# Performance work log

Measured on AMD Instinct MI355X. Metric: run time of the kernel, lower is better.

## Reference

```python
import jax, jax.numpy as jnp
import numpy as np

BN_EPS = 1e-5


def _conv2d(x, w, b, pad):
    # x: [B,C,H,W], w: [O,I,kh,kw] (OIHW)
    y = jax.lax.conv_general_dilated(
        x, w, window_strides=(1, 1), padding=[(pad, pad), (pad, pad)],
        dimension_numbers=('NCHW', 'OIHW', 'NCHW'))
    return y + b[None, :, None, None]


def setup_inputs() -> dict:
    key = jax.random.key(0)
    ks = jax.random.split(key, 4)
    B, C, D, H, W = 8, 256, 1, 64, 64
    dm = 256
    x = jax.random.normal(ks[0], (B, C, D, H, W), dtype=jnp.float32)
    wq = jax.random.normal(ks[1], (dm, dm, 1, 1), dtype=jnp.float32) * 0.05
    bq = jnp.zeros((dm,), jnp.float32)
    wkv = jax.random.normal(ks[2], (2 * dm, dm, 3, 3), dtype=jnp.float32) * 0.05
    bkv = jnp.zeros((2 * dm,), jnp.float32)
    gamma = jnp.ones((dm,), jnp.float32)
    beta = jnp.zeros((dm,), jnp.float32)
    return {"x": x, "wq": wq, "bq": bq, "wkv": wkv, "bkv": bkv,
            "gamma": gamma, "beta": beta}


def reference(x, wq, bq, wkv, bkv, gamma, beta):
    B = x.shape[0]
    H, W = x.shape[-2], x.shape[-1]
    xc = x.reshape(B, -1, H, W)            # 'b c d h w -> b (c d) h w'
    dm = xc.shape[1]
    q = jax.nn.relu(_conv2d(xc, wq, bq, 0))       # [B,dm,H,W]
    kv = jax.nn.relu(_conv2d(xc, wkv, bkv, 1))    # [B,2dm,H,W]
    k, v = jnp.split(kv, 2, axis=1)

    def tok(t):  # 'b c x y -> b (x y) c'
        return t.transpose(0, 2, 3, 1).reshape(B, H * W, dm)

    qt, kt, vt = tok(q), tok(k), tok(v)
    sim = jnp.einsum('bid,bjd->bij', qt, kt)       # [B,N,N]
    A = jax.nn.softmax(sim / jnp.sqrt(jnp.float32(dm)), axis=-1)
    r = jnp.einsum('bij,bjd->bid', A, vt)          # [B,N,dm]
    r = r.reshape(B, H, W, dm).transpose(0, 3, 1, 2)  # 'b (x y) c -> b c x y'
    y = r + xc
    # BatchNorm2d, training mode: batch stats over (B,H,W), biased variance
    mean = jnp.mean(y, axis=(0, 2, 3), keepdims=True)
    var = jnp.var(y, axis=(0, 2, 3), keepdims=True)
    out = (y - mean) * jax.lax.rsqrt(var + BN_EPS)
    out = out * gamma[None, :, None, None] + beta[None, :, None, None]
    return out
```

## Files before the change

### kernel.cpp

```cpp
#include <hip/hip_runtime.h>


typedef __attribute__((ext_vector_type(8))) short bf16x8;
typedef __attribute__((ext_vector_type(4))) float f32x4;
typedef __attribute__((ext_vector_type(8))) unsigned short u16x8;

__device__ inline unsigned short f2bf(float f) {
  union { float f; unsigned u; } c; c.f = f;
  unsigned u = c.u;
  return (unsigned short)((u + 0x7fffu + ((u >> 16) & 1u)) >> 16);
}

__device__ inline unsigned cvtpk(float lo, float hi) {
  unsigned r;
  asm("v_cvt_pk_bf16_f32 %0, %1, %2" : "=v"(r) : "v"(lo), "v"(hi));
  return r;
}

__device__ inline void dma16(const void* g, void* l) {
  __builtin_amdgcn_global_load_lds(
      (const __attribute__((address_space(1))) unsigned int*)g,
      (__attribute__((address_space(3))) unsigned int*)l, 16, 0, 0);
}

__global__ __launch_bounds__(256) void k_xt(
    const float* __restrict__ x, ushort* __restrict__ xt)
{
  const int b = blockIdx.z, ci0 = blockIdx.y * 64, gx = blockIdx.x;
  const int t = threadIdx.x;
  ushort* img = xt + (size_t)b * 4224 * 256;
  if (gx >= 64) {
    int r0 = (gx == 64) ? 0 : 4160;
#pragma unroll
    for (int k = 0; k < 2; ++k) {
      int idx = t + k * 256;
      int r = idx >> 3, u = idx & 7;
      u16x8 z = (u16x8)0;
      *(u16x8*)&img[(size_t)(r0 + r) * 256 + ci0 + u * 8] = z;
    }
    return;
  }
  const int n0 = gx * 64;
  __shared__ ushort tl[64][65];
  {
    const float* xb = x + ((size_t)b * 256 + ci0) * 4096 + n0;
    int i = t >> 2, j0 = (t & 3) * 16;
#pragma unroll
    for (int jj = 0; jj < 16; jj += 4) {
      float4 v = *(const float4*)&xb[(size_t)i * 4096 + j0 + jj];
      tl[j0 + jj + 0][i] = f2bf(v.x);
      tl[j0 + jj + 1][i] = f2bf(v.y);
      tl[j0 + jj + 2][i] = f2bf(v.z);
      tl[j0 + jj + 3][i] = f2bf(v.w);
    }
  }
  __syncthreads();
  {
    int j = t >> 3, u = t & 7;
#pragma unroll
    for (int k = 0; k < 2; ++k) {
      int jr = j + k * 32;
      ushort tmp[8];
#pragma unroll
      for (int e = 0; e < 8; ++e) tmp[e] = tl[jr][u * 8 + e];
      *(u16x8*)&img[(size_t)(64 + n0 + jr) * 256 + ci0 + u * 8] = *(u16x8*)tmp;
    }
  }
}

__global__ __launch_bounds__(256) void k_wprep(
    const float* __restrict__ w, ushort* __restrict__ wt, int ntaps, int nco)
{
  const int co = blockIdx.x;
  const int t = threadIdx.x;
  __shared__ float ws[2304];
  const int tot = 256 * ntaps;
  for (int i = t; i < tot; i += 256) ws[i] = w[(size_t)co * tot + i];
  __syncthreads();
  for (int tap = 0; tap < ntaps; ++tap)
    wt[((size_t)tap * nco + co) * 256 + t] = f2bf(ws[t * ntaps + tap]);
}

__global__ __launch_bounds__(256, 2) void k_conv(
    const ushort* __restrict__ xt, const ushort* __restrict__ wt,
    const float* __restrict__ bias, ushort* __restrict__ outT,
    ushort* __restrict__ outV, int ntaps, int nco, float oscale)
{
  extern __shared__ unsigned char smem[];
  ushort* As = (ushort*)smem;
  ushort* Bs = (ushort*)(smem + 20640);
  __shared__ float bias_s[256];

  const int t = threadIdx.x, lane = t & 63, wv = t >> 6;
  const int wm = wv >> 1, wn = wv & 1;
  const int qc = lane & 15, grp = lane >> 4;
  const int b = blockIdx.z, n0 = blockIdx.x * 128, co0 = blockIdx.y * 256;
  const bool nchw = (outV != nullptr) && (blockIdx.y == 1);
  const ushort* img = xt + (size_t)b * 4224 * 256 + (size_t)64 * 256;

  bias_s[t] = bias[co0 + t];

  f32x4 acc[4][8];
#pragma unroll
  for (int mi = 0; mi < 4; ++mi)
#pragma unroll
    for (int ni = 0; ni < 8; ++ni) acc[mi][ni] = f32x4{0.f, 0.f, 0.f, 0.f};

  for (int c8 = 0; c8 < 8; ++c8) {
    const int ci0 = c8 * 32;
    __syncthreads();
#pragma unroll
    for (int k = 0; k < 5; ++k) {
      int idx = t + k * 256;
      if (idx < 1032) {
        int r = idx >> 2, u = idx & 3;
        int n = n0 + r - 65;
        n = min(max(n, -64), 4159);
        u16x8 v = *(const u16x8*)&img[(size_t)n * 256 + ci0 + u * 8];
        *(u16x8*)&As[r * 40 + u * 8] = v;
      }
    }
    for (int tap = 0; tap < ntaps; ++tap) {
      const int dy = (ntaps == 9) ? (tap / 3 - 1) : 0;
      const int dx = (ntaps == 9) ? (tap % 3 - 1) : 0;
      const int off = dy * 64 + dx;
      __syncthreads();
      const ushort* wrow = wt + ((size_t)tap * nco + co0) * 256 + ci0;
#pragma unroll
      for (int k = 0; k < 4; ++k) {
        int idx = t + k * 256;
        int r = idx >> 2, u = idx & 3;
        *(u16x8*)&Bs[r * 40 + u * 8] = *(const u16x8*)&wrow[(size_t)r * 256 + u * 8];
      }
      __syncthreads();
      bf16x8 bf[8];
#pragma unroll
      for (int ni = 0; ni < 8; ++ni)
        bf[ni] = *(const bf16x8*)&Bs[(wn * 128 + ni * 16 + qc) * 40 + grp * 8];
#pragma unroll
      for (int mi = 0; mi < 4; ++mi) {
        int ar = wm * 64 + mi * 16 + qc + off + 65;
        bf16x8 af = *(const bf16x8*)&As[ar * 40 + grp * 8];
        if (dx < 0 && mi == 0 && qc == 0)  af = (bf16x8)0;
        if (dx > 0 && mi == 3 && qc == 15) af = (bf16x8)0;
#pragma unroll
        for (int ni = 0; ni < 8; ++ni)
          acc[mi][ni] = __builtin_amdgcn_mfma_f32_16x16x32_bf16(af, bf[ni], acc[mi][ni], 0, 0, 0);
      }
    }
  }

  __syncthreads();
  if (!nchw) {
    ushort (*olds)[264] = (ushort(*)[264])smem;
#pragma unroll
    for (int mi = 0; mi < 4; ++mi) {
      int p = wm * 64 + mi * 16 + grp * 4;
#pragma unroll
      for (int ni = 0; ni < 8; ++ni) {
        int c = wn * 128 + ni * 16 + qc;
        float bv = bias_s[c];
#pragma unroll
        for (int r = 0; r < 4; ++r)
          olds[p + r][c] = f2bf(fmaxf(acc[mi][ni][r] + bv, 0.f) * oscale);
      }
    }
    __syncthreads();
    ushort* dst = outT + ((size_t)b * 4096 + n0) * 256;
#pragma unroll
    for (int k = 0; k < 16; ++k) {
      int idx = t + k * 256;
      int r = idx >> 5, u = idx & 31;
      *(u16x8*)&dst[(size_t)r * 256 + u * 8] = *(const u16x8*)&olds[r][u * 8];
    }
  } else {
    ushort (*oldsT)[136] = (ushort(*)[136])smem;
#pragma unroll
    for (int mi = 0; mi < 4; ++mi) {
      int p = wm * 64 + mi * 16 + grp * 4;
#pragma unroll
      for (int ni = 0; ni < 8; ++ni) {
        int c = wn * 128 + ni * 16 + qc;
        float bv = bias_s[c];
        ushort4 pk;
        pk.x = f2bf(fmaxf(acc[mi][ni][0] + bv, 0.f) * oscale);
        pk.y = f2bf(fmaxf(acc[mi][ni][1] + bv, 0.f) * oscale);
        pk.z = f2bf(fmaxf(acc[mi][ni][2] + bv, 0.f) * oscale);
        pk.w = f2bf(fmaxf(acc[mi][ni][3] + bv, 0.f) * oscale);
        *(ushort4*)&oldsT[c][p] = pk;
      }
    }
    __syncthreads();
    ushort* dst = outV + (size_t)b * 256 * 4096 + n0;
#pragma unroll
    for (int k = 0; k < 16; ++k) {
      int idx = t + k * 256;
      int c = idx >> 4, u = idx & 15;
      *(u16x8*)&dst[(size_t)c * 4096 + u * 8] = *(const u16x8*)&oldsT[c][u * 8];
    }
  }
}

__global__ __launch_bounds__(512, 2) void k_attn(
    const ushort* __restrict__ q_t, const ushort* __restrict__ k_t,
    const ushort* __restrict__ v_t, const float* __restrict__ x,
    float* __restrict__ y, float* __restrict__ gstat)
{
  extern __shared__ unsigned char smem[];
  ushort* kbf0 = (ushort*)smem;
  ushort* kbf1 = (ushort*)(smem + 32768);
  ushort* vbf0 = (ushort*)(smem + 65536);
  ushort* vbf1 = (ushort*)(smem + 98304);
  ushort* pl   = (ushort*)(smem + 131072);

  const int tid = threadIdx.x, lane = tid & 63, w = tid >> 6;
  const int grp = lane >> 4, qc = lane & 15, xr = qc & 7;
  const int b = blockIdx.y, q0 = blockIdx.x * 128;
  const int wbase = tid & ~63;

  int offk[4], offv[4];
#pragma unroll
  for (int k = 0; k < 4; ++k) {
    int i = k * 512 + tid;
    int j = i >> 5, s = i & 31;
    offk[k] = j * 256 + ((s ^ (j & 7)) << 3);
    int d = i >> 3, s2 = i & 7;
    offv[k] = d * 4096 + ((s2 ^ (d & 7)) << 3);
  }
  const ushort* kT = k_t + (size_t)b * 4096 * 256;
  const ushort* vT = v_t + (size_t)b * 256 * 4096;

  bf16x8 qf[8];
  {
    const ushort* qrow = q_t + ((size_t)b * 4096 + q0 + w * 16 + qc) * 256;
#pragma unroll
    for (int dc = 0; dc < 8; ++dc)
      qf[dc] = *(const bf16x8*)&qrow[dc * 32 + grp * 8];
  }

  f32x4 o[16];
#pragma unroll
  for (int dt = 0; dt < 16; ++dt) o[dt] = f32x4{0.f, 0.f, 0.f, 0.f};
  float m_run = -1e30f, lp = 0.f;

  auto stage = [&](const ushort* kp, const ushort* vp, ushort* kb, ushort* vb) {
#pragma unroll
    for (int k = 0; k < 4; ++k)
      dma16(kp + offk[k], kb + (size_t)(k * 512 + wbase) * 8);
#pragma unroll
    for (int k = 0; k < 4; ++k)
      dma16(vp + offv[k], vb + (size_t)(k * 512 + wbase) * 8);
  };

  stage(kT, vT, kbf0, vbf0);
  kT += 16384; vT += 64;
  asm volatile("s_waitcnt vmcnt(0)" ::: "memory");
  __syncthreads();

  ushort* prow = pl + (size_t)(w * 16 + qc) * 64;
  int po[4], pslot[2];
#pragma unroll
  for (int kt = 0; kt < 4; ++kt)
    po[kt] = (((2 * kt + (grp >> 1)) ^ xr) << 3) + ((grp & 1) << 2);
#pragma unroll
  for (int kc = 0; kc < 2; ++kc)
    pslot[kc] = ((kc * 4 + grp) ^ xr) << 3;

  for (int t = 0; t < 64; ++t) {
    ushort* kb = (t & 1) ? kbf1 : kbf0;
    ushort* vb = (t & 1) ? vbf1 : vbf0;
    if (t < 63) {
      stage(kT, vT, (t & 1) ? kbf0 : kbf1, (t & 1) ? vbf0 : vbf1);
      kT += 16384; vT += 64;
    }

    f32x4 st[4];
    __builtin_amdgcn_s_setprio(1);
#pragma unroll
    for (int kt = 0; kt < 4; ++kt) {
      const int row = (kt * 16 + qc) * 256;
      bf16x8 ka8[8];
#pragma unroll
      for (int dc = 0; dc < 8; ++dc)
        ka8[dc] = *(const bf16x8*)&kb[row + (((dc * 4 + grp) ^ xr) << 3)];
      f32x4 a = f32x4{0.f, 0.f, 0.f, 0.f};
#pragma unroll
      for (int dc = 0; dc < 8; ++dc)
        a = __builtin_amdgcn_mfma_f32_16x16x32_bf16(ka8[dc], qf[dc], a, 0, 0, 0);
      st[kt] = a;
    }
    __builtin_amdgcn_s_setprio(0);

    float pmax = fmaxf(
        fmaxf(fmaxf(st[0][0], st[0][1]), fmaxf(st[0][2], st[0][3])),
        fmaxf(fmaxf(st[1][0], st[1][1]), fmaxf(st[1][2], st[1][3])));
    pmax = fmaxf(pmax, fmaxf(
        fmaxf(fmaxf(st[2][0], st[2][1]), fmaxf(st[2][2], st[2][3])),
        fmaxf(fmaxf(st[3][0], st[3][1]), fmaxf(st[3][2], st[3][3]))));
    pmax = fmaxf(pmax, __shfl_xor(pmax, 16));
    pmax = fmaxf(pmax, __shfl_xor(pmax, 32));
    if (pmax - m_run > 11.5f) {
      float mn = fmaxf(m_run, pmax);
      float al = exp2f(m_run - mn);
      m_run = mn; lp *= al;
#pragma unroll
      for (int dt = 0; dt < 16; ++dt) {
        o[dt][0] *= al; o[dt][1] *= al; o[dt][2] *= al; o[dt][3] *= al;
      }
    }
#pragma unroll
    for (int kt = 0; kt < 4; ++kt) {
      float p0 = exp2f(st[kt][0] - m_run);
      float p1 = exp2f(st[kt][1] - m_run);
      float p2 = exp2f(st[kt][2] - m_run);
      float p3 = exp2f(st[kt][3] - m_run);
      lp += (p0 + p1) + (p2 + p3);
      uint2 pk = { cvtpk(p0, p1), cvtpk(p2, p3) };
      *(uint2*)&prow[po[kt]] = pk;
    }

    bf16x8 pb0 = *(const bf16x8*)&prow[pslot[0]];
    bf16x8 pb1 = *(const bf16x8*)&prow[pslot[1]];
    bf16x8 vaA[8], vaB[8];
#pragma unroll
    for (int j = 0; j < 8; ++j) {
      int dt = j >> 1;
      vaA[j] = *(const bf16x8*)&vb[(dt * 16 + qc) * 64 + pslot[j & 1]];
    }
    __builtin_amdgcn_s_setprio(1);
#pragma unroll
    for (int bt = 0; bt < 4; ++bt) {
      const bf16x8* cur = (bt & 1) ? vaB : vaA;
      bf16x8* nxt = (bt & 1) ? vaA : vaB;
      if (bt < 3) {
#pragma unroll
        for (int j = 0; j < 8; ++j) {
          int dt = (bt + 1) * 4 + (j >> 1);
          nxt[j] = *(const bf16x8*)&vb[(dt * 16 + qc) * 64 + pslot[j & 1]];
        }
      }
#pragma unroll
      for (int j2 = 0; j2 < 4; ++j2) {
        int dt = bt * 4 + j2;
        o[dt] = __builtin_amdgcn_mfma_f32_16x16x32_bf16(cur[2 * j2],     pb0, o[dt], 0, 0, 0);
        o[dt] = __builtin_amdgcn_mfma_f32_16x16x32_bf16(cur[2 * j2 + 1], pb1, o[dt], 0, 0, 0);
      }
    }
    __builtin_amdgcn_s_setprio(0);

    asm volatile("s_waitcnt vmcnt(0)" ::: "memory");
    __syncthreads();
  }

  lp += __shfl_xor(lp, 16);
  lp += __shfl_xor(lp, 32);
  float inv = 1.f / lp;

  float (*obuf)[132] = (float(*)[132])smem;
  float* bnacc = (float*)(smem + 135168);
  bnacc[tid] = 0.f;
#pragma unroll
  for (int dt = 0; dt < 16; ++dt)
#pragma unroll
    for (int r = 0; r < 4; ++r)
      obuf[dt * 16 + grp * 4 + r][w * 16 + qc] = o[dt][r] * inv;
  __syncthreads();

  const float* xb = x + (size_t)b * 256 * 4096 + q0;
  float*       yb = y + (size_t)b * 256 * 4096 + q0;
  for (int i = tid; i < 8192; i += 512) {
    int c = i >> 5, f4 = (i & 31) << 2;
    float4 xr4 = *(const float4*)&xb[(size_t)c * 4096 + f4];
    float4 rv = *(const float4*)&obuf[c][f4];
    rv.x += xr4.x; rv.y += xr4.y; rv.z += xr4.z; rv.w += xr4.w;
    *(float4*)&yb[(size_t)c * 4096 + f4] = rv;
    float ls1 = (rv.x + rv.y) + (rv.z + rv.w);
    float ls2 = (rv.x * rv.x + rv.y * rv.y) + (rv.z * rv.z + rv.w * rv.w);
    atomicAdd(&bnacc[c], ls1);
    atomicAdd(&bnacc[256 + c], ls2);
  }
  __syncthreads();
  if (tid < 256) {
    atomicAdd(&gstat[tid], bnacc[tid]);
    atomicAdd(&gstat[256 + tid], bnacc[256 + tid]);
  }
}

__global__ __launch_bounds__(256) void k_bnfin(
    const float* __restrict__ gstat, const float* __restrict__ gamma,
    const float* __restrict__ beta, float* __restrict__ scale,
    float* __restrict__ shift)
{
  const int c = threadIdx.x;
  float mean = gstat[c] * (1.f / 32768.f);
  float var  = gstat[256 + c] * (1.f / 32768.f) - mean * mean;
  float inv  = rsqrtf(var + 1e-5f);
  float g = gamma[c] * inv;
  scale[c] = g;
  shift[c] = beta[c] - mean * g;
}

__global__ __launch_bounds__(256) void k_bnapply(
    float* __restrict__ y, const float* __restrict__ scale,
    const float* __restrict__ shift)
{
  const int total4 = 8 * 256 * 1024;
  for (int i = blockIdx.x * 256 + threadIdx.x; i < total4; i += gridDim.x * 256) {
    int c = (i >> 10) & 255;
    float sc = scale[c], sh = shift[c];
    float4 v = ((const float4*)y)[i];
    v.x = fmaf(v.x, sc, sh);
    v.y = fmaf(v.y, sc, sh);
    v.z = fmaf(v.z, sc, sh);
    v.w = fmaf(v.w, sc, sh);
    ((float4*)y)[i] = v;
  }
}

extern "C" void kernel_launch(void* const* d_in, const int* in_sizes, int n_in,
                              void* d_out, int out_size, void* d_ws, size_t ws_size,
                              hipStream_t stream) {
  const float* x     = (const float*)d_in[0];
  const float* wq    = (const float*)d_in[1];
  const float* bq    = (const float*)d_in[2];
  const float* wkv   = (const float*)d_in[3];
  const float* bkv   = (const float*)d_in[4];
  const float* gamma = (const float*)d_in[5];
  const float* beta  = (const float*)d_in[6];
  float* out = (float*)d_out;

  ushort* xt  = (ushort*)d_ws;
  ushort* wt3 = xt  + (size_t)8650752;
  ushort* wt1 = wt3 + (size_t)1179648;
  ushort* q_t = wt1 + (size_t)65536;
  ushort* k_t = q_t + (size_t)8388608;
  ushort* v_t = k_t + (size_t)8388608;
  float* scale = (float*)(v_t + (size_t)8388608);
  float* shift = scale + 256;
  float* gstat = shift + 256;

  hipMemsetAsync(gstat, 0, 2048, stream);

  k_xt<<<dim3(66, 4, 8), 256, 0, stream>>>(x, xt);
  k_wprep<<<dim3(512), 256, 0, stream>>>(wkv, wt3, 9, 512);
  k_wprep<<<dim3(256), 256, 0, stream>>>(wq, wt1, 1, 256);

  const int conv_smem = 69632;
  hipFuncSetAttribute(reinterpret_cast<const void*>(k_conv),
                      hipFuncAttributeMaxDynamicSharedMemorySize, conv_smem);
  k_conv<<<dim3(32, 1, 8), 256, conv_smem, stream>>>(
      xt, wt1, bq, q_t, nullptr, 1, 256, 0.0625f * 1.44269504f);
  k_conv<<<dim3(32, 2, 8), 256, conv_smem, stream>>>(
      xt, wt3, bkv, k_t, v_t, 9, 512, 1.0f);

  const int attn_smem = 147456;
  hipFuncSetAttribute(reinterpret_cast<const void*>(k_attn),
                      hipFuncAttributeMaxDynamicSharedMemorySize, attn_smem);
  k_attn<<<dim3(32, 8), 512, attn_smem, stream>>>(q_t, k_t, v_t, x, out, gstat);

  k_bnfin<<<dim3(1), 256, 0, stream>>>(gstat, gamma, beta, scale, shift);
  k_bnapply<<<dim3(2048), 256, 0, stream>>>(out, scale, shift);
}
```

Measured before the change: 332.6 us.

## Double-buffer conv tiles via direct LDS DMA, simplify attention loads, warp-reduce BN stats

The conv kernel now stages input and weight tiles with global_load_lds DMA into double-buffered LDS with unpadded rows, prefetching the next tap or channel chunk while the current one computes. This drops one of the two barriers per tap. The attention kernel replaces explicit K and V register prefetch arrays with inline per-MFMA LDS loads, which lowers register pressure but exposes more load latency. The BN statistics move from LDS atomics to a shuffle reduction followed by per-32-lane global atomics, which raises global atomic traffic. Unpadded 32-element rows may cause LDS bank conflicts on the fragment reads.

```diff
diff --git a/kernel.cpp b/kernel.cpp
--- a/kernel.cpp
+++ b/kernel.cpp
@@ -87,16 +87,19 @@
     ushort* __restrict__ outV, int ntaps, int nco, float oscale)
 {
   extern __shared__ unsigned char smem[];
-  ushort* As = (ushort*)smem;
-  ushort* Bs = (ushort*)(smem + 20640);
+  ushort* As0 = (ushort*)smem;
+  ushort* As1 = (ushort*)(smem + 16512);
+  ushort* Bs0 = (ushort*)(smem + 33024);
+  ushort* Bs1 = (ushort*)(smem + 33024 + 16384);
   __shared__ float bias_s[256];
 
-  const int t = threadIdx.x, lane = t & 63, wv = t >> 6;
-  const int wm = wv >> 1, wn = wv & 1;
+  const int t = threadIdx.x, lane = t & 63;
+  const int wv = t >> 6, wm = wv >> 1, wn = wv & 1;
   const int qc = lane & 15, grp = lane >> 4;
   const int b = blockIdx.z, n0 = blockIdx.x * 128, co0 = blockIdx.y * 256;
   const bool nchw = (outV != nullptr) && (blockIdx.y == 1);
   const ushort* img = xt + (size_t)b * 4224 * 256 + (size_t)64 * 256;
+  const int wbase = t & ~63;
 
   bias_s[t] = bias[co0 + t];
 
@@ -106,51 +109,69 @@
 #pragma unroll
     for (int ni = 0; ni < 8; ++ni) acc[mi][ni] = f32x4{0.f, 0.f, 0.f, 0.f};
 
-  for (int c8 = 0; c8 < 8; ++c8) {
+  auto stageA = [&](int c8, ushort* dst) {
     const int ci0 = c8 * 32;
-    __syncthreads();
 #pragma unroll
     for (int k = 0; k < 5; ++k) {
-      int idx = t + k * 256;
+      int idx = k * 256 + t;
       if (idx < 1032) {
         int r = idx >> 2, u = idx & 3;
-        int n = n0 + r - 65;
-        n = min(max(n, -64), 4159);
-        u16x8 v = *(const u16x8*)&img[(size_t)n * 256 + ci0 + u * 8];
-        *(u16x8*)&As[r * 40 + u * 8] = v;
-      }
-    }
-    for (int tap = 0; tap < ntaps; ++tap) {
+        int n = min(max(n0 + r - 65, -64), 4159);
+        dma16(img + (size_t)n * 256 + ci0 + u * 8,
+              dst + (size_t)(k * 256 + wbase) * 8);
+      }
+    }
+  };
+  auto stageB = [&](int tap, int c8, ushort* dst) {
+    const ushort* wrow = wt + ((size_t)tap * nco + co0) * 256 + c8 * 32;
+#pragma unroll
+    for (int k = 0; k < 4; ++k) {
+      int idx = k * 256 + t;
+      int r = idx >> 2, u = idx & 3;
+      dma16(wrow + (size_t)r * 256 + u * 8,
+            dst + (size_t)(k * 256 + wbase) * 8);
+    }
+  };
+
+  stageA(0, As0);
+  stageB(0, 0, Bs0);
+  asm volatile("s_waitcnt vmcnt(0)" ::: "memory");
+  __syncthreads();
+
+  const int niters = 8 * ntaps;
+  int iter = 0;
+  for (int c8 = 0; c8 < 8; ++c8) {
+    const ushort* Asb = (c8 & 1) ? As1 : As0;
+    for (int tap = 0; tap < ntaps; ++tap, ++iter) {
+      const ushort* Bsb = (iter & 1) ? Bs1 : Bs0;
+      if (iter + 1 < niters) {
+        int ntap = (tap + 1 == ntaps) ? 0 : tap + 1;
+        int nc8  = (tap + 1 == ntaps) ? c8 + 1 : c8;
+        stageB(ntap, nc8, (iter & 1) ? Bs0 : Bs1);
+        if (ntap == 0) stageA(nc8, (c8 & 1) ? As0 : As1);
+      }
       const int dy = (ntaps == 9) ? (tap / 3 - 1) : 0;
       const int dx = (ntaps == 9) ? (tap % 3 - 1) : 0;
       const int off = dy * 64 + dx;
-      __syncthreads();
-      const ushort* wrow = wt + ((size_t)tap * nco + co0) * 256 + ci0;
-#pragma unroll
-      for (int k = 0; k < 4; ++k) {
-        int idx = t + k * 256;
-        int r = idx >> 2, u = idx & 3;
-        *(u16x8*)&Bs[r * 40 + u * 8] = *(const u16x8*)&wrow[(size_t)r * 256 + u * 8];
-      }
-      __syncthreads();
       bf16x8 bf[8];
 #pragma unroll
       for (int ni = 0; ni < 8; ++ni)
-        bf[ni] = *(const bf16x8*)&Bs[(wn * 128 + ni * 16 + qc) * 40 + grp * 8];
+        bf[ni] = *(const bf16x8*)&Bsb[(wn * 128 + ni * 16 + qc) * 32 + grp * 8];
 #pragma unroll
       for (int mi = 0; mi < 4; ++mi) {
         int ar = wm * 64 + mi * 16 + qc + off + 65;
-        bf16x8 af = *(const bf16x8*)&As[ar * 40 + grp * 8];
+        bf16x8 af = *(const bf16x8*)&Asb[ar * 32 + grp * 8];
         if (dx < 0 && mi == 0 && qc == 0)  af = (bf16x8)0;
         if (dx > 0 && mi == 3 && qc == 15) af = (bf16x8)0;
 #pragma unroll
         for (int ni = 0; ni < 8; ++ni)
           acc[mi][ni] = __builtin_amdgcn_mfma_f32_16x16x32_bf16(af, bf[ni], acc[mi][ni], 0, 0, 0);
       }
-    }
-  }
-
-  __syncthreads();
+      asm volatile("s_waitcnt vmcnt(0)" ::: "memory");
+      __syncthreads();
+    }
+  }
+
   if (!nchw) {
     ushort (*olds)[264] = (ushort(*)[264])smem;
 #pragma unroll
@@ -279,14 +300,12 @@
 #pragma unroll
     for (int kt = 0; kt < 4; ++kt) {
       const int row = (kt * 16 + qc) * 256;
-      bf16x8 ka8[8];
-#pragma unroll
-      for (int dc = 0; dc < 8; ++dc)
-        ka8[dc] = *(const bf16x8*)&kb[row + (((dc * 4 + grp) ^ xr) << 3)];
       f32x4 a = f32x4{0.f, 0.f, 0.f, 0.f};
 #pragma unroll
-      for (int dc = 0; dc < 8; ++dc)
-        a = __builtin_amdgcn_mfma_f32_16x16x32_bf16(ka8[dc], qf[dc], a, 0, 0, 0);
+      for (int dc = 0; dc < 8; ++dc) {
+        bf16x8 ka = *(const bf16x8*)&kb[row + (((dc * 4 + grp) ^ xr) << 3)];
+        a = __builtin_amdgcn_mfma_f32_16x16x32_bf16(ka, qf[dc], a, 0, 0, 0);
+      }
       st[kt] = a;
     }
     __builtin_amdgcn_s_setprio(0);
@@ -321,30 +340,14 @@
 
     bf16x8 pb0 = *(const bf16x8*)&prow[pslot[0]];
     bf16x8 pb1 = *(const bf16x8*)&prow[pslot[1]];
-    bf16x8 vaA[8], vaB[8];
-#pragma unroll
-    for (int j = 0; j < 8; ++j) {
-      int dt = j >> 1;
-      vaA[j] = *(const bf16x8*)&vb[(dt * 16 + qc) * 64 + pslot[j & 1]];
-    }
     __builtin_amdgcn_s_setprio(1);
 #pragma unroll
-    for (int bt = 0; bt < 4; ++bt) {
-      const bf16x8* cur = (bt & 1) ? vaB : vaA;
-      bf16x8* nxt = (bt & 1) ? vaA : vaB;
-      if (bt < 3) {
-#pragma unroll
-        for (int j = 0; j < 8; ++j) {
-          int dt = (bt + 1) * 4 + (j >> 1);
-          nxt[j] = *(const bf16x8*)&vb[(dt * 16 + qc) * 64 + pslot[j & 1]];
-        }
-      }
-#pragma unroll
-      for (int j2 = 0; j2 < 4; ++j2) {
-        int dt = bt * 4 + j2;
-        o[dt] = __builtin_amdgcn_mfma_f32_16x16x32_bf16(cur[2 * j2],     pb0, o[dt], 0, 0, 0);
-        o[dt] = __builtin_amdgcn_mfma_f32_16x16x32_bf16(cur[2 * j2 + 1], pb1, o[dt], 0, 0, 0);
-      }
+    for (int dt = 0; dt < 16; ++dt) {
+      const int vrow = (dt * 16 + qc) * 64;
+      bf16x8 va0 = *(const bf16x8*)&vb[vrow + pslot[0]];
+      bf16x8 va1 = *(const bf16x8*)&vb[vrow + pslot[1]];
+      o[dt] = __builtin_amdgcn_mfma_f32_16x16x32_bf16(va0, pb0, o[dt], 0, 0, 0);
+      o[dt] = __builtin_amdgcn_mfma_f32_16x16x32_bf16(va1, pb1, o[dt], 0, 0, 0);
     }
     __builtin_amdgcn_s_setprio(0);
 
@@ -357,8 +360,6 @@
   float inv = 1.f / lp;
 
   float (*obuf)[132] = (float(*)[132])smem;
-  float* bnacc = (float*)(smem + 135168);
-  bnacc[tid] = 0.f;
 #pragma unroll
   for (int dt = 0; dt < 16; ++dt)
 #pragma unroll
@@ -376,13 +377,15 @@
     *(float4*)&yb[(size_t)c * 4096 + f4] = rv;
     float ls1 = (rv.x + rv.y) + (rv.z + rv.w);
     float ls2 = (rv.x * rv.x + rv.y * rv.y) + (rv.z * rv.z + rv.w * rv.w);
-    atomicAdd(&bnacc[c], ls1);
-    atomicAdd(&bnacc[256 + c], ls2);
-  }
-  __syncthreads();
-  if (tid < 256) {
-    atomicAdd(&gstat[tid], bnacc[tid]);
-    atomicAdd(&gstat[256 + tid], bnacc[256 + tid]);
+#pragma unroll
+    for (int sh = 1; sh <= 16; sh <<= 1) {
+      ls1 += __shfl_xor(ls1, sh);
+      ls2 += __shfl_xor(ls2, sh);
+    }
+    if ((tid & 31) == 0) {
+      atomicAdd(&gstat[c], ls1);
+      atomicAdd(&gstat[256 + c], ls2);
+    }
   }
 }
 
```

Result: slower. 381.6 us (+14.7%).
